# Kernel tuning notes

Measured on AMD Instinct MI355X. Metric: run time of the kernel, lower is better.

Reference implementation:

```python
import jax, jax.numpy as jnp
import numpy as np

N, C_IN, C_OUT, H, W = 8, 128, 64, 128, 128
KH, KW, DILATE = 9, 9, 2


def _shifted(xp, dh, dw, dilate, Hh, Ww):
    # xp: zero-padded [N,C,H+2ph,W+2pw]; returns window-offset (dh,dw) view [N,C,H,W]
    return xp[:, :, dh * dilate:dh * dilate + Hh, dw * dilate:dw * dilate + Ww]


def local_similar(q, k, kH, kW, dilate):
    # q,k: [N,C,H,W] -> logits [N,H,W,kH*kW]
    n, c, h, w = q.shape
    ph, pw = dilate * (kH // 2), dilate * (kW // 2)
    kp = jnp.pad(k, ((0, 0), (0, 0), (ph, ph), (pw, pw)))
    outs = []
    for dh in range(kH):
        for dw in range(kW):
            ks = _shifted(kp, dh, dw, dilate, h, w)
            outs.append(jnp.einsum('nchw,nchw->nhw', q, ks))
    return jnp.stack(outs, axis=-1)


def local_weighting(v, wgt, kH, kW, dilate):
    # v: [N,C,H,W], wgt: [N,H,W,kH*kW] -> [N,C,H,W]
    n, c, h, w = v.shape
    ph, pw = dilate * (kH // 2), dilate * (kW // 2)
    vp = jnp.pad(v, ((0, 0), (0, 0), (ph, ph), (pw, pw)))
    out = jnp.zeros_like(v)
    idx = 0
    for dh in range(kH):
        for dw in range(kW):
            vs = _shifted(vp, dh, dw, dilate, h, w)
            out = out + vs * wgt[..., idx][:, None, :, :]
            idx += 1
    return out


def setup_inputs() -> dict:
    key = jax.random.key(0)
    kx, k1, k2, k3 = jax.random.split(key, 4)
    s = 1.0 / np.sqrt(C_IN)
    return {
        'x': jax.random.normal(kx, (N, C_IN, H, W), dtype=jnp.float32),
        'W1': jax.random.normal(k1, (C_OUT, C_IN), dtype=jnp.float32) * s,
        'W2': jax.random.normal(k2, (C_OUT, C_IN), dtype=jnp.float32) * s,
        'W3': jax.random.normal(k3, (C_OUT, C_IN), dtype=jnp.float32) * s,
    }


def reference(x, W1, W2, W3):
    # 1x1 convs (no bias)
    x1 = jnp.einsum('oc,nchw->nohw', W1, x)
    x2 = jnp.einsum('oc,nchw->nohw', W2, x)
    x3 = jnp.einsum('oc,nchw->nohw', W3, x)
    logits = local_similar(x1, x2, KH, KW, DILATE)      # [N,H,W,kH*kW]
    weight = jax.nn.softmax(logits, axis=-1)
    out = local_weighting(x3, weight, KH, KW, DILATE)   # [N,C_out,H,W]
    return out
```

## Files before the change

### kernel.cpp

```cpp
#include <hip/hip_runtime.h>
#include <cstdint>
#include <cstddef>

#define NB   8
#define CIN  128
#define COUT 64
#define NPIX 131072
#define PLANE NPIX
#define LOG2E 1.44269504088896340736f

typedef _Float16 f16;
typedef _Float16 half4_t __attribute__((ext_vector_type(4)));
typedef _Float16 half8_t __attribute__((ext_vector_type(8)));
typedef short    bs8    __attribute__((ext_vector_type(8)));
typedef float    float4_t __attribute__((ext_vector_type(4)));
typedef unsigned int uint2_t __attribute__((ext_vector_type(2)));

__device__ __forceinline__ unsigned short f2bf(float f){
  unsigned u = __float_as_uint(f);
  return (unsigned short)((u + 0x7fffu + ((u >> 16) & 1u)) >> 16);
}

__global__ __launch_bounds__(256, 4) void conv_mfma_k(
    const float* __restrict__ x,
    const float* __restrict__ W1, const float* __restrict__ W2,
    const float* __restrict__ W3,
    f16* __restrict__ Qi, f16* __restrict__ Ki, unsigned short* __restrict__ V2)
{
  __shared__ __align__(16) f16 xs[64 * 136];

  int tid = threadIdx.x, lane = tid & 63, wv = tid >> 6;
  int l15 = lane & 15, q4 = lane >> 4;
  int b = blockIdx.x;
  int vb = (b & 7) * 256 + (b >> 3);
  int pxt = vb * 64;
  int n = pxt >> 14, hwt = pxt & 16383;

  half8_t wq[4], wk[4], wvf[4];
  #pragma unroll
  for (int k0 = 0; k0 < 4; ++k0) {
    int rb = (wv * 16 + l15) * 128 + k0 * 32 + q4 * 8;
    float4_t a0 = *(const float4_t*)&W1[rb];
    float4_t a1 = *(const float4_t*)&W1[rb + 4];
    float4_t b0 = *(const float4_t*)&W2[rb];
    float4_t b1 = *(const float4_t*)&W2[rb + 4];
    float4_t c0 = *(const float4_t*)&W3[rb];
    float4_t c1 = *(const float4_t*)&W3[rb + 4];
    #pragma unroll
    for (int j = 0; j < 4; ++j) {
      wq[k0][j]      = (f16)(a0[j] * LOG2E);
      wq[k0][j + 4]  = (f16)(a1[j] * LOG2E);
      wk[k0][j]      = (f16)b0[j];
      wk[k0][j + 4]  = (f16)b1[j];
      wvf[k0][j]     = (f16)c0[j];
      wvf[k0][j + 4] = (f16)c1[j];
    }
  }

  {
    const float* xp = x + ((size_t)(n * CIN + wv * 32) << 14) + hwt + lane;
    #pragma unroll
    for (int c0 = 0; c0 < 32; c0 += 8) {
      half8_t hh;
      #pragma unroll
      for (int j = 0; j < 8; ++j)
        hh[j] = (f16)xp[(size_t)(c0 + j) << 14];
      *(half8_t*)&xs[lane * 136 + wv * 32 + c0] = hh;
    }
  }
  __syncthreads();

  #pragma unroll
  for (int mt = 0; mt < 4; ++mt) {
    float4_t cq = {0.f,0.f,0.f,0.f}, ck = {0.f,0.f,0.f,0.f}, cv = {0.f,0.f,0.f,0.f};
    #pragma unroll
    for (int k0 = 0; k0 < 4; ++k0) {
      half8_t xa = *(half8_t*)&xs[(mt*16 + l15)*136 + k0*32 + q4*8];
      cq = __builtin_amdgcn_mfma_f32_16x16x32_f16(wq[k0],  xa, cq, 0, 0, 0);
      ck = __builtin_amdgcn_mfma_f32_16x16x32_f16(wk[k0],  xa, ck, 0, 0, 0);
      cv = __builtin_amdgcn_mfma_f32_16x16x32_f16(xa, wvf[k0], cv, 0, 0, 0);
    }
    int pxq = pxt + mt*16 + l15;
    int g   = wv*2 + (q4 >> 1);
    half4_t hq = {(f16)cq[0], (f16)cq[1], (f16)cq[2], (f16)cq[3]};
    half4_t hk = {(f16)ck[0], (f16)ck[1], (f16)ck[2], (f16)ck[3]};
    *(half4_t*)&Qi[((size_t)g * PLANE + pxq) * 8 + (q4 & 1)*4] = hq;
    *(half4_t*)&Ki[((size_t)g * PLANE + pxq) * 8 + (q4 & 1)*4] = hk;
    uint2_t pv;
    pv.x = (unsigned)f2bf(cv[0]) | ((unsigned)f2bf(cv[1]) << 16);
    pv.y = (unsigned)f2bf(cv[2]) | ((unsigned)f2bf(cv[3]) << 16);
    *(uint2_t*)&V2[(size_t)(wv*16 + l15) * PLANE + pxt + mt*16 + q4*4] = pv;
  }
}

__global__ __launch_bounds__(512, 4) void attn_fused_k(
    const f16* __restrict__ Qi, const f16* __restrict__ Ki,
    const unsigned short* __restrict__ V2, float* __restrict__ out)
{
  __shared__ __align__(16) unsigned short plds[8][2][16 * 40];

  int tid = threadIdx.x, lane = tid & 63, wv = tid >> 6;
  int l15 = lane & 15, q4 = lane >> 4;
  int b = blockIdx.x;
  int n = b & 7;
  int p = b >> 3;
  int h0 = (p >> 1)*4 + (p & 1);
  int h2 = h0 + 2;
  int seg = wv * 16;
  int nb = n << 14;

  unsigned short* P0 = &plds[wv][0][0];
  unsigned short* P1 = &plds[wv][1][0];

  half8_t aq0[2], aq1[2];
  {
    int px0 = nb + (h0 << 7) + seg + l15;
    aq0[0] = *(const half8_t*)&Qi[((size_t)(q4    ) * PLANE + px0) * 8];
    aq0[1] = *(const half8_t*)&Qi[((size_t)(q4 + 4) * PLANE + px0) * 8];
    int px1 = px0 + 256;
    aq1[0] = *(const half8_t*)&Qi[((size_t)(q4    ) * PLANE + px1) * 8];
    aq1[1] = *(const half8_t*)&Qi[((size_t)(q4 + 4) * PLANE + px1) * 8];
  }

  unsigned vbits = 0;
  #pragma unroll
  for (int jt = 0; jt < 2; ++jt)
    #pragma unroll
    for (int rr = 0; rr < 4; ++rr) {
      int jw = seg - 8 + jt*16 + q4*4 + rr;
      int iw = seg + l15;
      int d  = jw - iw;
      bool val = (((d & 1) == 0) & (d >= -8) & (d <= 8) & ((unsigned)jw < 128u));
      vbits |= ((unsigned)val) << (jt*4 + rr);
    }

  float s0 = 0.f, s1 = 0.f;
  float4_t o0[4], o1[4];
  #pragma unroll
  for (int ct = 0; ct < 4; ++ct) {
    o0[ct] = (float4_t){0.f,0.f,0.f,0.f};
    o1[ct] = (float4_t){0.f,0.f,0.f,0.f};
  }

  auto row_body = [&](const half8_t* aq, float& s_part,
                      float4_t* o, unsigned short* P,
                      const half8_t (&bk)[2][2], const bs8 (&bv)[4]) {
    float4_t st0 = (float4_t){0.f,0.f,0.f,0.f};
    float4_t st1 = (float4_t){0.f,0.f,0.f,0.f};
    st0 = __builtin_amdgcn_mfma_f32_16x16x32_f16(bk[0][0], aq[0], st0, 0, 0, 0);
    st0 = __builtin_amdgcn_mfma_f32_16x16x32_f16(bk[0][1], aq[1], st0, 0, 0, 0);
    st1 = __builtin_amdgcn_mfma_f32_16x16x32_f16(bk[1][0], aq[0], st1, 0, 0, 0);
    st1 = __builtin_amdgcn_mfma_f32_16x16x32_f16(bk[1][1], aq[1], st1, 0, 0, 0);
    #pragma unroll
    for (int rr = 0; rr < 4; ++rr) {
      st0[rr] = exp2f(((vbits >> rr)       & 1u) ? st0[rr] : -1e30f);
      st1[rr] = exp2f(((vbits >> (4 + rr)) & 1u) ? st1[rr] : -1e30f);
    }
    s_part += (st0[0] + st0[1]) + (st0[2] + st0[3])
            + (st1[0] + st1[1]) + (st1[2] + st1[3]);
    uint2_t pk0, pk1;
    pk0.x = (__float_as_uint(st0[1]) & 0xffff0000u) | (__float_as_uint(st0[0]) >> 16);
    pk0.y = (__float_as_uint(st0[3]) & 0xffff0000u) | (__float_as_uint(st0[2]) >> 16);
    pk1.x = (__float_as_uint(st1[1]) & 0xffff0000u) | (__float_as_uint(st1[0]) >> 16);
    pk1.y = (__float_as_uint(st1[3]) & 0xffff0000u) | (__float_as_uint(st1[2]) >> 16);
    *(uint2_t*)&P[l15*40      + q4*4] = pk0;
    *(uint2_t*)&P[l15*40 + 16 + q4*4] = pk1;
    bs8 ap = *(bs8*)&P[l15*40 + q4*8];
    #pragma unroll
    for (int ct = 0; ct < 4; ++ct)
      o[ct] = __builtin_amdgcn_mfma_f32_16x16x32_bf16(ap, bv[ct], o[ct], 0, 0, 0);
  };

  for (int hs = h0 - 8; hs <= h0 + 10; hs += 2) {
    if (hs < 0 || hs > 127) continue;
    int jbase = nb + (hs << 7) + seg - 8;

    half8_t bk[2][2];
    #pragma unroll
    for (int jt = 0; jt < 2; ++jt) {
      int pxj = jbase + jt*16 + l15;
      bk[jt][0] = *(const half8_t*)&Ki[((size_t)(q4    ) * PLANE + pxj) * 8];
      bk[jt][1] = *(const half8_t*)&Ki[((size_t)(q4 + 4) * PLANE + pxj) * 8];
    }
    bs8 bv[4];
    #pragma unroll
    for (int ct = 0; ct < 4; ++ct)
      bv[ct] = *(const bs8*)&V2[(size_t)(ct*16 + l15) * PLANE + jbase + q4*8];

    if (hs <= h0 + 8) row_body(aq0, s0, o0, P0, bk, bv);
    if (hs >= h2 - 8) row_body(aq1, s1, o1, P1, bk, bv);
  }

  int iw = seg + l15;
  int wlo = iw - 8; if (wlo < 0) wlo = 0;
  int whi = iw + 8; if (whi > 127) whi = 127;
  int vw = ((whi - wlo) >> 1) + 1;
  #pragma unroll
  for (int row = 0; row < 2; ++row) {
    int hr = row ? h2 : h0;
    int hlo = hr - 8; if (hlo < 0) hlo = 0;
    int hhi = hr + 8; if (hhi > 127) hhi = 127;
    int vh = ((hhi - hlo) >> 1) + 1;
    float cnt = (float)(81 - vh * vw);
    float srow = row ? s1 : s0;
    srow += __shfl_xor(srow, 16, 64);
    srow += __shfl_xor(srow, 32, 64);
    float sc = 1.f / (srow + cnt);
    float4_t scv;
    #pragma unroll
    for (int rr = 0; rr < 4; ++rr) scv[rr] = __shfl(sc, q4*4 + rr, 64);
    const float4_t* o = row ? o1 : o0;
    #pragma unroll
    for (int ct = 0; ct < 4; ++ct) {
      size_t ob = ((size_t)(n*COUT + ct*16 + l15) << 14) + (hr << 7) + seg + q4*4;
      float4_t stv;
      #pragma unroll
      for (int rr = 0; rr < 4; ++rr) stv[rr] = o[ct][rr] * scv[rr];
      *(float4_t*)&out[ob] = stv;
    }
  }
}

extern "C" void kernel_launch(void* const* d_in, const int* in_sizes, int n_in,
                              void* d_out, int out_size, void* d_ws, size_t ws_size,
                              hipStream_t stream)
{
  const float* x  = (const float*)d_in[0];
  const float* W1 = (const float*)d_in[1];
  const float* W2 = (const float*)d_in[2];
  const float* W3 = (const float*)d_in[3];

  f16* Qi = (f16*)((char*)d_ws + 65536);
  f16* Ki = Qi + (size_t)8 * PLANE * 8;
  unsigned short* V2 = (unsigned short*)(Ki + (size_t)8 * PLANE * 8);

  float* outp = (float*)d_out;

  conv_mfma_k <<<NPIX/64,  256, 0, stream>>>(x, W1, W2, W3, Qi, Ki, V2);
  attn_fused_k<<<NB*128/2, 512, 0, stream>>>(Qi, Ki, V2, outp);
}
```

Baseline: 166.3 us.

## Fuse 1x1 projection convs into attention kernel, recomputing K/V per block in LDS

Replaces the separate projection kernel and its global Q/K/V buffers with a single kernel. Each block stages x rows into shared memory and computes Q for its two output rows and K/V for every needed source row on the fly. This removes the intermediate writes and reads and one launch. In exchange it recomputes K/V redundantly across neighbouring blocks, re-reads x many times, adds many block barriers and uses about 63KB of LDS, which limits occupancy.

```diff
diff --git a/kernel.cpp b/kernel.cpp
--- a/kernel.cpp
+++ b/kernel.cpp
@@ -5,8 +5,6 @@
 #define NB   8
 #define CIN  128
 #define COUT 64
-#define NPIX 131072
-#define PLANE NPIX
 #define LOG2E 1.44269504088896340736f
 
 typedef _Float16 f16;
@@ -21,83 +19,17 @@
   return (unsigned short)((u + 0x7fffu + ((u >> 16) & 1u)) >> 16);
 }
 
-__global__ __launch_bounds__(256, 4) void conv_mfma_k(
-    const float* __restrict__ x,
-    const float* __restrict__ W1, const float* __restrict__ W2,
-    const float* __restrict__ W3,
-    f16* __restrict__ Qi, f16* __restrict__ Ki, unsigned short* __restrict__ V2)
+__global__ __launch_bounds__(512, 4) void fused_k(
+    const float* __restrict__ x, const float* __restrict__ W1,
+    const float* __restrict__ W2, const float* __restrict__ W3,
+    float* __restrict__ out)
 {
-  __shared__ __align__(16) f16 xs[64 * 136];
-
-  int tid = threadIdx.x, lane = tid & 63, wv = tid >> 6;
-  int l15 = lane & 15, q4 = lane >> 4;
-  int b = blockIdx.x;
-  int vb = (b & 7) * 256 + (b >> 3);
-  int pxt = vb * 64;
-  int n = pxt >> 14, hwt = pxt & 16383;
-
-  half8_t wq[4], wk[4], wvf[4];
-  #pragma unroll
-  for (int k0 = 0; k0 < 4; ++k0) {
-    int rb = (wv * 16 + l15) * 128 + k0 * 32 + q4 * 8;
-    float4_t a0 = *(const float4_t*)&W1[rb];
-    float4_t a1 = *(const float4_t*)&W1[rb + 4];
-    float4_t b0 = *(const float4_t*)&W2[rb];
-    float4_t b1 = *(const float4_t*)&W2[rb + 4];
-    float4_t c0 = *(const float4_t*)&W3[rb];
-    float4_t c1 = *(const float4_t*)&W3[rb + 4];
-    #pragma unroll
-    for (int j = 0; j < 4; ++j) {
-      wq[k0][j]      = (f16)(a0[j] * LOG2E);
-      wq[k0][j + 4]  = (f16)(a1[j] * LOG2E);
-      wk[k0][j]      = (f16)b0[j];
-      wk[k0][j + 4]  = (f16)b1[j];
-      wvf[k0][j]     = (f16)c0[j];
-      wvf[k0][j + 4] = (f16)c1[j];
-    }
-  }
-
-  {
-    const float* xp = x + ((size_t)(n * CIN + wv * 32) << 14) + hwt + lane;
-    #pragma unroll
-    for (int c0 = 0; c0 < 32; c0 += 8) {
-      half8_t hh;
-      #pragma unroll
-      for (int j = 0; j < 8; ++j)
-        hh[j] = (f16)xp[(size_t)(c0 + j) << 14];
-      *(half8_t*)&xs[lane * 136 + wv * 32 + c0] = hh;
-    }
-  }
-  __syncthreads();
-
-  #pragma unroll
-  for (int mt = 0; mt < 4; ++mt) {
-    float4_t cq = {0.f,0.f,0.f,0.f}, ck = {0.f,0.f,0.f,0.f}, cv = {0.f,0.f,0.f,0.f};
-    #pragma unroll
-    for (int k0 = 0; k0 < 4; ++k0) {
-      half8_t xa = *(half8_t*)&xs[(mt*16 + l15)*136 + k0*32 + q4*8];
-      cq = __builtin_amdgcn_mfma_f32_16x16x32_f16(wq[k0],  xa, cq, 0, 0, 0);
-      ck = __builtin_amdgcn_mfma_f32_16x16x32_f16(wk[k0],  xa, ck, 0, 0, 0);
-      cv = __builtin_amdgcn_mfma_f32_16x16x32_f16(xa, wvf[k0], cv, 0, 0, 0);
-    }
-    int pxq = pxt + mt*16 + l15;
-    int g   = wv*2 + (q4 >> 1);
-    half4_t hq = {(f16)cq[0], (f16)cq[1], (f16)cq[2], (f16)cq[3]};
-    half4_t hk = {(f16)ck[0], (f16)ck[1], (f16)ck[2], (f16)ck[3]};
-    *(half4_t*)&Qi[((size_t)g * PLANE + pxq) * 8 + (q4 & 1)*4] = hq;
-    *(half4_t*)&Ki[((size_t)g * PLANE + pxq) * 8 + (q4 & 1)*4] = hk;
-    uint2_t pv;
-    pv.x = (unsigned)f2bf(cv[0]) | ((unsigned)f2bf(cv[1]) << 16);
-    pv.y = (unsigned)f2bf(cv[2]) | ((unsigned)f2bf(cv[3]) << 16);
-    *(uint2_t*)&V2[(size_t)(wv*16 + l15) * PLANE + pxt + mt*16 + q4*4] = pv;
-  }
-}
-
-__global__ __launch_bounds__(512, 4) void attn_fused_k(
-    const f16* __restrict__ Qi, const f16* __restrict__ Ki,
-    const unsigned short* __restrict__ V2, float* __restrict__ out)
-{
-  __shared__ __align__(16) unsigned short plds[8][2][16 * 40];
+  __shared__ __align__(16) unsigned char smem[64512];
+  f16* xs = (f16*)smem;
+  f16* Kl = (f16*)(smem + 17408);
+  unsigned short* Vl = (unsigned short*)(smem + 35840);
+  unsigned short* plds = (unsigned short*)(smem + 54272);
+  f16* Ql = (f16*)(smem + 35840);
 
   int tid = threadIdx.x, lane = tid & 63, wv = tid >> 6;
   int l15 = lane & 15, q4 = lane >> 4;
@@ -107,31 +39,100 @@
   int h0 = (p >> 1)*4 + (p & 1);
   int h2 = h0 + 2;
   int seg = wv * 16;
-  int nb = n << 14;
-
-  unsigned short* P0 = &plds[wv][0][0];
-  unsigned short* P1 = &plds[wv][1][0];
+
+  int strip = wv & 3;
+  const float* Wkv = (wv >= 4) ? W3 : W2;
+  half8_t wf[4];
+  #pragma unroll
+  for (int k0 = 0; k0 < 4; ++k0) {
+    int rb = (strip*16 + l15)*128 + k0*32 + q4*8;
+    float4_t f0 = *(const float4_t*)&Wkv[rb];
+    float4_t f1 = *(const float4_t*)&Wkv[rb + 4];
+    #pragma unroll
+    for (int j = 0; j < 4; ++j) { wf[k0][j] = (f16)f0[j]; wf[k0][j+4] = (f16)f1[j]; }
+  }
+
+  auto stage64 = [&](int row, int c) {
+    int c4 = tid >> 4, pg = tid & 15;
+    const float* xp = x + ((size_t)(n * CIN + c4 * 4) << 14) + (row << 7) + c * 64 + pg * 4;
+    float4_t v0 = *(const float4_t*)xp;
+    float4_t v1 = *(const float4_t*)(xp + 16384);
+    float4_t v2 = *(const float4_t*)(xp + 32768);
+    float4_t v3 = *(const float4_t*)(xp + 49152);
+    #pragma unroll
+    for (int i = 0; i < 4; ++i) {
+      half4_t h = {(f16)v0[i], (f16)v1[i], (f16)v2[i], (f16)v3[i]};
+      *(half4_t*)&xs[(pg * 4 + i) * 136 + c4 * 4] = h;
+    }
+  };
 
   half8_t aq0[2], aq1[2];
-  {
-    int px0 = nb + (h0 << 7) + seg + l15;
-    aq0[0] = *(const half8_t*)&Qi[((size_t)(q4    ) * PLANE + px0) * 8];
-    aq0[1] = *(const half8_t*)&Qi[((size_t)(q4 + 4) * PLANE + px0) * 8];
-    int px1 = px0 + 256;
-    aq1[0] = *(const half8_t*)&Qi[((size_t)(q4    ) * PLANE + px1) * 8];
-    aq1[1] = *(const half8_t*)&Qi[((size_t)(q4 + 4) * PLANE + px1) * 8];
+  #pragma unroll
+  for (int rr = 0; rr < 2; ++rr) {
+    int row = rr ? h2 : h0;
+    #pragma unroll
+    for (int c = 0; c < 2; ++c) {
+      __syncthreads();
+      stage64(row, c);
+      __syncthreads();
+      if ((wv >> 2) == c) {
+        int mt = wv & 3;
+        #pragma unroll
+        for (int s = 0; s < 4; ++s) {
+          half8_t wq[4];
+          #pragma unroll
+          for (int k0 = 0; k0 < 4; ++k0) {
+            int rb = (s*16 + l15)*128 + k0*32 + q4*8;
+            float4_t f0 = *(const float4_t*)&W1[rb];
+            float4_t f1 = *(const float4_t*)&W1[rb + 4];
+            #pragma unroll
+            for (int j = 0; j < 4; ++j) {
+              wq[k0][j]   = (f16)(f0[j] * LOG2E);
+              wq[k0][j+4] = (f16)(f1[j] * LOG2E);
+            }
+          }
+          float4_t a = {0.f,0.f,0.f,0.f};
+          #pragma unroll
+          for (int k0 = 0; k0 < 4; ++k0) {
+            half8_t xa = *(half8_t*)&xs[(mt*16 + l15)*136 + k0*32 + q4*8];
+            a = __builtin_amdgcn_mfma_f32_16x16x32_f16(wq[k0], xa, a, 0, 0, 0);
+          }
+          int g = s*2 + (q4 >> 1);
+          int px = wv*16 + l15;
+          half4_t h = {(f16)a[0], (f16)a[1], (f16)a[2], (f16)a[3]};
+          *(half4_t*)&Ql[(size_t)(g*128 + px)*8 + (q4 & 1)*4] = h;
+        }
+      }
+    }
+    __syncthreads();
+    half8_t a0 = *(half8_t*)&Ql[(size_t)((q4    )*128 + seg + l15)*8];
+    half8_t a1 = *(half8_t*)&Ql[(size_t)((q4 + 4)*128 + seg + l15)*8];
+    if (rr == 0) { aq0[0] = a0; aq0[1] = a1; }
+    else         { aq1[0] = a0; aq1[1] = a1; }
+  }
+  __syncthreads();
+
+  if (tid < 128) {
+    int g = tid >> 4, hp = tid & 15;
+    int idx = (hp < 8) ? hp : 128 + hp;
+    *(float4_t*)&Kl[(size_t)(g*144 + idx)*8] = (float4_t){0.f,0.f,0.f,0.f};
+  }
+  if (tid < 128) {
+    int row = tid >> 1;
+    int idx = (tid & 1) ? 136 : 0;
+    *(float4_t*)&Vl[(size_t)row*144 + idx] = (float4_t){0.f,0.f,0.f,0.f};
   }
 
   unsigned vbits = 0;
   #pragma unroll
   for (int jt = 0; jt < 2; ++jt)
     #pragma unroll
-    for (int rr = 0; rr < 4; ++rr) {
-      int jw = seg - 8 + jt*16 + q4*4 + rr;
+    for (int rrr = 0; rrr < 4; ++rrr) {
+      int jw = seg - 8 + jt*16 + q4*4 + rrr;
       int iw = seg + l15;
       int d  = jw - iw;
       bool val = (((d & 1) == 0) & (d >= -8) & (d <= 8) & ((unsigned)jw < 128u));
-      vbits |= ((unsigned)val) << (jt*4 + rr);
+      vbits |= ((unsigned)val) << (jt*4 + rrr);
     }
 
   float s0 = 0.f, s1 = 0.f;
@@ -142,8 +143,9 @@
     o1[ct] = (float4_t){0.f,0.f,0.f,0.f};
   }
 
-  auto row_body = [&](const half8_t* aq, float& s_part,
-                      float4_t* o, unsigned short* P,
+  unsigned short* P = plds + wv * 640;
+
+  auto row_body = [&](const half8_t* aq, float& s_part, float4_t* o,
                       const half8_t (&bk)[2][2], const bs8 (&bv)[4]) {
     float4_t st0 = (float4_t){0.f,0.f,0.f,0.f};
     float4_t st1 = (float4_t){0.f,0.f,0.f,0.f};
@@ -152,9 +154,9 @@
     st1 = __builtin_amdgcn_mfma_f32_16x16x32_f16(bk[1][0], aq[0], st1, 0, 0, 0);
     st1 = __builtin_amdgcn_mfma_f32_16x16x32_f16(bk[1][1], aq[1], st1, 0, 0, 0);
     #pragma unroll
-    for (int rr = 0; rr < 4; ++rr) {
-      st0[rr] = exp2f(((vbits >> rr)       & 1u) ? st0[rr] : -1e30f);
-      st1[rr] = exp2f(((vbits >> (4 + rr)) & 1u) ? st1[rr] : -1e30f);
+    for (int r = 0; r < 4; ++r) {
+      st0[r] = exp2f(((vbits >> r)       & 1u) ? st0[r] : -1e30f);
+      st1[r] = exp2f(((vbits >> (4 + r)) & 1u) ? st1[r] : -1e30f);
     }
     s_part += (st0[0] + st0[1]) + (st0[2] + st0[3])
             + (st1[0] + st1[1]) + (st1[2] + st1[3]);
@@ -173,22 +175,57 @@
 
   for (int hs = h0 - 8; hs <= h0 + 10; hs += 2) {
     if (hs < 0 || hs > 127) continue;
-    int jbase = nb + (hs << 7) + seg - 8;
+
+    #pragma unroll
+    for (int c = 0; c < 2; ++c) {
+      __syncthreads();
+      stage64(hs, c);
+      __syncthreads();
+      if (wv < 4) {
+        #pragma unroll
+        for (int mt = 0; mt < 4; ++mt) {
+          float4_t a = {0.f,0.f,0.f,0.f};
+          #pragma unroll
+          for (int k0 = 0; k0 < 4; ++k0) {
+            half8_t xa = *(half8_t*)&xs[(mt*16 + l15)*136 + k0*32 + q4*8];
+            a = __builtin_amdgcn_mfma_f32_16x16x32_f16(wf[k0], xa, a, 0, 0, 0);
+          }
+          int px = c*64 + mt*16 + l15;
+          int g = strip*2 + (q4 >> 1);
+          half4_t h = {(f16)a[0], (f16)a[1], (f16)a[2], (f16)a[3]};
+          *(half4_t*)&Kl[(size_t)(g*144 + 8 + px)*8 + (q4 & 1)*4] = h;
+        }
+      } else {
+        #pragma unroll
+        for (int mt = 0; mt < 4; ++mt) {
+          float4_t a = {0.f,0.f,0.f,0.f};
+          #pragma unroll
+          for (int k0 = 0; k0 < 4; ++k0) {
+            half8_t xa = *(half8_t*)&xs[(mt*16 + l15)*136 + k0*32 + q4*8];
+            a = __builtin_amdgcn_mfma_f32_16x16x32_f16(xa, wf[k0], a, 0, 0, 0);
+          }
+          uint2_t pv;
+          pv.x = (unsigned)f2bf(a[0]) | ((unsigned)f2bf(a[1]) << 16);
+          pv.y = (unsigned)f2bf(a[2]) | ((unsigned)f2bf(a[3]) << 16);
+          *(uint2_t*)&Vl[(size_t)(strip*16 + l15)*144 + 8 + c*64 + mt*16 + q4*4] = pv;
+        }
+      }
+    }
+    __syncthreads();
 
     half8_t bk[2][2];
     #pragma unroll
     for (int jt = 0; jt < 2; ++jt) {
-      int pxj = jbase + jt*16 + l15;
-      bk[jt][0] = *(const half8_t*)&Ki[((size_t)(q4    ) * PLANE + pxj) * 8];
-      bk[jt][1] = *(const half8_t*)&Ki[((size_t)(q4 + 4) * PLANE + pxj) * 8];
+      bk[jt][0] = *(half8_t*)&Kl[(size_t)((q4    )*144 + seg + jt*16 + l15)*8];
+      bk[jt][1] = *(half8_t*)&Kl[(size_t)((q4 + 4)*144 + seg + jt*16 + l15)*8];
     }
     bs8 bv[4];
     #pragma unroll
     for (int ct = 0; ct < 4; ++ct)
-      bv[ct] = *(const bs8*)&V2[(size_t)(ct*16 + l15) * PLANE + jbase + q4*8];
-
-    if (hs <= h0 + 8) row_body(aq0, s0, o0, P0, bk, bv);
-    if (hs >= h2 - 8) row_body(aq1, s1, o1, P1, bk, bv);
+      bv[ct] = *(bs8*)&Vl[(size_t)(ct*16 + l15)*144 + seg + q4*8];
+
+    if (hs <= h0 + 8) row_body(aq0, s0, o0, bk, bv);
+    if (hs >= h2 - 8) row_body(aq1, s1, o1, bk, bv);
   }
 
   int iw = seg + l15;
@@ -208,14 +245,14 @@
     float sc = 1.f / (srow + cnt);
     float4_t scv;
     #pragma unroll
-    for (int rr = 0; rr < 4; ++rr) scv[rr] = __shfl(sc, q4*4 + rr, 64);
+    for (int r = 0; r < 4; ++r) scv[r] = __shfl(sc, q4*4 + r, 64);
     const float4_t* o = row ? o1 : o0;
     #pragma unroll
     for (int ct = 0; ct < 4; ++ct) {
       size_t ob = ((size_t)(n*COUT + ct*16 + l15) << 14) + (hr << 7) + seg + q4*4;
       float4_t stv;
       #pragma unroll
-      for (int rr = 0; rr < 4; ++rr) stv[rr] = o[ct][rr] * scv[rr];
+      for (int r = 0; r < 4; ++r) stv[r] = o[ct][r] * scv[r];
       *(float4_t*)&out[ob] = stv;
     }
   }
@@ -229,13 +266,8 @@
   const float* W1 = (const float*)d_in[1];
   const float* W2 = (const float*)d_in[2];
   const float* W3 = (const float*)d_in[3];
-
-  f16* Qi = (f16*)((char*)d_ws + 65536);
-  f16* Ki = Qi + (size_t)8 * PLANE * 8;
-  unsigned short* V2 = (unsigned short*)(Ki + (size_t)8 * PLANE * 8);
-
   float* outp = (float*)d_out;
-
-  conv_mfma_k <<<NPIX/64,  256, 0, stream>>>(x, W1, W2, W3, Qi, Ki, V2);
-  attn_fused_k<<<NB*128/2, 512, 0, stream>>>(Qi, Ki, V2, outp);
+  (void)d_ws; (void)ws_size;
+
+  fused_k<<<NB * 128 / 2, 512, 0, stream>>>(x, W1, W2, W3, outp);
 }
```

New measurement: 194.1 us. 16.7% more time.
